# Performance work log

Hardware: AMD Instinct MI355X
Metric: run time of the kernel (lower is better)

## Reference

```python
import jax, jax.numpy as jnp
import numpy as np

B, C, H, W = 4, 128, 64, 64


def setup_inputs() -> dict:
    key = jax.random.key(0)
    ks = jax.random.split(key, 7)
    s = 1.0 / np.sqrt(C)
    return {
        "x": jax.random.normal(ks[0], (B, C, H, W), dtype=jnp.float32),
        "Wq": jax.random.normal(ks[1], (C, C), dtype=jnp.float32) * s,
        "bq": jnp.zeros((C,), dtype=jnp.float32),
        "Wk": jax.random.normal(ks[2], (C, C), dtype=jnp.float32) * s,
        "bk": jnp.zeros((C,), dtype=jnp.float32),
        "Wv": jax.random.normal(ks[3], (C, C), dtype=jnp.float32) * s,
        "bv": jnp.zeros((C,), dtype=jnp.float32),
    }


def reference(x, Wq, bq, Wk, bk, Wv, bv):
    b, c, h, w = x.shape
    n = h * w
    scale = c ** (-0.5)
    # tokens: [B, N, C]
    xt = x.reshape(b, c, n).transpose(0, 2, 1)
    # 1x1 convs == per-token channel GEMMs (out[c'] = sum_c W[c',c] x[c] + b[c'])
    q = jnp.einsum("bnc,dc->bnd", xt, Wq) + bq  # [B, N, C]
    k = jnp.einsum("bnc,dc->bnd", xt, Wk) + bk  # [B, N, C]
    v = jnp.einsum("bnc,dc->bnd", xt, Wv) + bv  # [B, N, C]
    scores = jnp.einsum("bic,bjc->bij", q, k) * scale  # [B, N, N]
    attn = jax.nn.softmax(scores, axis=-1)
    out = jnp.einsum("bij,bjc->bic", attn, v)  # [B, N, C]
    return out.transpose(0, 2, 1).reshape(b, c, h, w)
```

## Files before the change

kernel.cpp:

```cpp
#include <hip/hip_runtime.h>
#include <hip/hip_bf16.h>


#define BATCH 4
#define CH    128
#define NTOK  4096
#define TK    64
#define SCALE 0.08838834764831845f
#define LOG2E 1.4426950408889634f
#define MFIX  16.0f

typedef __attribute__((ext_vector_type(8)))  short short8;
typedef __attribute__((ext_vector_type(4)))  float f32x4;
typedef __attribute__((ext_vector_type(16))) float f32x16;

static __device__ __forceinline__ unsigned short f2bf(float f) {
    __hip_bfloat16 h = (__hip_bfloat16)f;
    return *(const unsigned short*)&h;
}

static __device__ __forceinline__ unsigned cvt_pk_bf16(float lo, float hi) {
    unsigned r;
    asm("v_cvt_pk_bf16_f32 %0, %1, %2" : "=v"(r) : "v"(lo), "v"(hi));
    return r;
}

static __device__ __forceinline__ short8 pack_bf16x8(float4 a, float4 b) {
    union { unsigned u[4]; short8 s8; } f;
    f.u[0] = cvt_pk_bf16(a.x, a.y);
    f.u[1] = cvt_pk_bf16(a.z, a.w);
    f.u[2] = cvt_pk_bf16(b.x, b.y);
    f.u[3] = cvt_pk_bf16(b.z, b.w);
    return f.s8;
}

__global__ __launch_bounds__(256) void proj_mfma_kernel(
    const float* __restrict__ x,
    const float* __restrict__ Wq, const float* __restrict__ Wk,
    const float* __restrict__ Wv,
    const float* __restrict__ bq, const float* __restrict__ bk,
    const float* __restrict__ bv,
    unsigned short* __restrict__ q_ws, unsigned short* __restrict__ kf_ws,
    unsigned short* __restrict__ vt_ws)
{
    __shared__ __align__(16) unsigned short Wl[CH * CH];
    __shared__ __align__(16) unsigned short XsT[64 * CH];

    const int t    = threadIdx.x;
    const int w    = t >> 6;
    const int lane = t & 63;
    const int quad = lane >> 4;
    const int c16  = lane & 15;
    const int n0   = blockIdx.x * 64;
    const int b    = blockIdx.y;
    const int z    = blockIdx.z;
    const float* xb = x + (size_t)b * CH * NTOK;
    const float* wm = (z == 0) ? Wq : (z == 1) ? Wk : Wv;

    #pragma unroll
    for (int i = 0; i < 8; ++i) {
        const int f   = i * 256 + t;
        const int row = f >> 4;
        const int u   = f & 15;
        const float* src = wm + f * 8;
        const float4 a = *(const float4*)src;
        const float4 c = *(const float4*)(src + 4);
        *(short8*)&Wl[row * CH + ((u ^ (row & 15)) << 3)] = pack_bf16x8(a, c);
    }
    {
        const int tok = lane;
        #pragma unroll
        for (int cc = 0; cc < 4; ++cc) {
            const int cb = 32 * w + 8 * cc;
            float xv[8];
            #pragma unroll
            for (int j = 0; j < 8; ++j)
                xv[j] = xb[(size_t)(cb + j) * NTOK + n0 + tok];
            union { unsigned u[4]; short8 s8; } pk;
            #pragma unroll
            for (int j = 0; j < 4; ++j)
                pk.u[j] = cvt_pk_bf16(xv[2 * j], xv[2 * j + 1]);
            const int phys = ((cb >> 3) ^ (tok & 15));
            *(short8*)&XsT[tok * CH + phys * 8] = pk.s8;
        }
    }
    __syncthreads();

    if (z < 2) {
        const float* bias = (z == 0) ? bq : bk;
        const float mul = (z == 0) ? (SCALE * LOG2E) : 1.0f;
        short8 xa[4];
        #pragma unroll
        for (int ks = 0; ks < 4; ++ks)
            xa[ks] = *(const short8*)&XsT[(16 * w + c16) * CH + (((4 * ks + quad) ^ c16) << 3)];
        #pragma unroll
        for (int nt = 0; nt < 8; ++nt) {
            f32x4 a = (f32x4){0.f, 0.f, 0.f, 0.f};
            #pragma unroll
            for (int ks = 0; ks < 4; ++ks) {
                const short8 bf = *(const short8*)
                    &Wl[(16 * nt + c16) * CH + (((4 * ks + quad) ^ c16) << 3)];
                a = __builtin_amdgcn_mfma_f32_16x16x32_bf16(xa[ks], bf, a, 0, 0, 0);
            }
            const float bvv = bias[16 * nt + c16];
            #pragma unroll
            for (int r = 0; r < 4; ++r) {
                const int n = n0 + 16 * w + quad * 4 + r;
                if (z == 0) {
                    q_ws[((size_t)b * NTOK + n) * CH + 16 * nt + c16] =
                        f2bf((a[r] + bvv) * mul);
                } else {
                    const size_t idx =
                        (((size_t)b * (NTOK >> 5) + (n >> 5)) * 8 + nt) * 512
                        + ((n & 31) + 32 * (c16 >> 3)) * 8 + (c16 & 7);
                    kf_ws[idx] = f2bf(a[r] + bvv);
                }
            }
        }
    } else {
        #pragma unroll
        for (int nt = 0; nt < 4; ++nt) {
            short8 xbf[4];
            #pragma unroll
            for (int ks = 0; ks < 4; ++ks)
                xbf[ks] = *(const short8*)&XsT[(16 * nt + c16) * CH + (((4 * ks + quad) ^ c16) << 3)];
            #pragma unroll
            for (int mt = 0; mt < 2; ++mt) {
                const int crow16 = 16 * (2 * w + mt);
                f32x4 acc = (f32x4){0.f, 0.f, 0.f, 0.f};
                #pragma unroll
                for (int ks = 0; ks < 4; ++ks) {
                    const short8 wva = *(const short8*)
                        &Wl[(crow16 + c16) * CH + (((4 * ks + quad) ^ c16) << 3)];
                    acc = __builtin_amdgcn_mfma_f32_16x16x32_bf16(wva, xbf[ks], acc, 0, 0, 0);
                }
                #pragma unroll
                for (int r = 0; r < 4; ++r) {
                    const int crow = crow16 + quad * 4 + r;
                    vt_ws[((size_t)b * CH + crow) * NTOK + n0 + 16 * nt + c16] =
                        f2bf(acc[r] + bv[crow]);
                }
            }
        }
    }
}

template <int SPLIT>
__global__ __launch_bounds__(256, 2) void flash_attn_mfma(
    const unsigned short* __restrict__ q_ws,
    const unsigned short* __restrict__ kf_ws,
    const unsigned short* __restrict__ vt_ws,
    float* __restrict__ out,
    float* __restrict__ Op, float* __restrict__ l_p)
{
    __shared__ __align__(16) unsigned short VtU[2][CH * TK];

    const int t    = threadIdx.x;
    const int w    = t >> 6;
    const int lane = t & 63;
    const int half = lane >> 5;
    const int l32  = lane & 31;
    const int jc   = blockIdx.y;
    const int b    = blockIdx.z;
    const int n0   = blockIdx.x * 128;
    const int jbeg = jc * (NTOK / SPLIT);
    constexpr int NT = (NTOK / SPLIT) / TK;
    static_assert(NT >= 2, "need at least 2 tiles");

    const unsigned short* kg = kf_ws + (size_t)b * NTOK * CH;
    const unsigned short* vg = vt_ws + (size_t)b * CH * NTOK;

    short8 qa[8];
    {
        const unsigned short* qrow =
            q_ws + ((size_t)b * NTOK + n0 + 32 * w + l32) * CH;
        #pragma unroll
        for (int ks = 0; ks < 8; ++ks)
            qa[ks] = *(const short8*)(qrow + ks * 16 + half * 8);
    }

    f32x16 Oa[4];
    #pragma unroll
    for (int ct = 0; ct < 4; ++ct) Oa[ct] = (f32x16)(0.0f);
    float lsum = 0.f;

    const int vcl = lane >> 3, vu = lane & 7;

    auto V_DMA = [&](int buf, int jj) {
        #pragma unroll
        for (int ci = 0; ci < 4; ++ci) {
            const int c = 32 * w + 8 * ci + vcl;
            const int g = vu ^ (c & 7);
            const unsigned short* src = vg + (size_t)c * NTOK + jj + g * 8;
            __builtin_amdgcn_global_load_lds(
                (const __attribute__((address_space(1))) void*)src,
                (__attribute__((address_space(3))) void*)&VtU[buf][(32 * w + 8 * ci) * TK],
                16, 0, 0);
        }
    };

    short8 kf[2][8];
    auto KF_LOAD = [&](int jj) {
        const unsigned short* kb = kg + (size_t)(jj >> 5) * 8 * 512;
        #pragma unroll
        for (int kt = 0; kt < 2; ++kt)
            #pragma unroll
            for (int ks = 0; ks < 8; ++ks)
                kf[kt][ks] = *(const short8*)(kb + ((kt * 8 + ks) * 64 + lane) * 8);
    };

    V_DMA(0, jbeg);
    KF_LOAD(jbeg);

    int j0 = jbeg;
    for (int tt = 0; tt < NT; ++tt, j0 += TK) {
        const int cur = tt & 1;
        if (tt + 1 < NT) {
            V_DMA(cur ^ 1, j0 + TK);
            asm volatile("s_waitcnt vmcnt(8)" ::: "memory");
        } else {
            asm volatile("s_waitcnt vmcnt(0)" ::: "memory");
        }
        __builtin_amdgcn_sched_barrier(0);
        __builtin_amdgcn_s_barrier();
        __builtin_amdgcn_sched_barrier(0);

        f32x16 s[2];
        s[0] = (f32x16)(-MFIX);
        s[1] = (f32x16)(-MFIX);
        #pragma unroll
        for (int ks = 0; ks < 8; ++ks) {
            s[0] = __builtin_amdgcn_mfma_f32_32x32x16_bf16(kf[0][ks], qa[ks], s[0], 0, 0, 0);
            s[1] = __builtin_amdgcn_mfma_f32_32x32x16_bf16(kf[1][ks], qa[ks], s[1], 0, 0, 0);
        }
        __builtin_amdgcn_sched_barrier(0);
        if (tt + 1 < NT) KF_LOAD(j0 + TK);
        __builtin_amdgcn_sched_barrier(0);

        short8 pb[4];
        #pragma unroll
        for (int kt = 0; kt < 2; ++kt) {
            float p[16];
            #pragma unroll
            for (int r = 0; r < 16; ++r) p[r] = exp2f(s[kt][r]);
            float a0 = 0.f, a1 = 0.f, a2 = 0.f, a3 = 0.f;
            #pragma unroll
            for (int r = 0; r < 4; ++r) {
                a0 += p[r]; a1 += p[4 + r]; a2 += p[8 + r]; a3 += p[12 + r];
            }
            lsum += (a0 + a1) + (a2 + a3);
            unsigned wd[8];
            #pragma unroll
            for (int i = 0; i < 8; ++i) wd[i] = cvt_pk_bf16(p[2 * i], p[2 * i + 1]);
            auto r02 = __builtin_amdgcn_permlane32_swap(wd[0], wd[2], false, false);
            auto r13 = __builtin_amdgcn_permlane32_swap(wd[1], wd[3], false, false);
            auto r46 = __builtin_amdgcn_permlane32_swap(wd[4], wd[6], false, false);
            auto r57 = __builtin_amdgcn_permlane32_swap(wd[5], wd[7], false, false);
            union { unsigned u[4]; short8 s8; } f0, f1;
            f0.u[0] = r02[0]; f0.u[1] = r13[0]; f0.u[2] = r02[1]; f0.u[3] = r13[1];
            f1.u[0] = r46[0]; f1.u[1] = r57[0]; f1.u[2] = r46[1]; f1.u[3] = r57[1];
            pb[2 * kt + 0] = f0.s8;
            pb[2 * kt + 1] = f1.s8;
        }

        #pragma unroll
        for (int ks2 = 0; ks2 < 4; ++ks2) {
            #pragma unroll
            for (int ct = 0; ct < 4; ++ct) {
                const int ch = 32 * ct + l32;
                const int ph = (2 * ks2 + half) ^ (ch & 7);
                const short8 vf = *(const short8*)&VtU[cur][ch * TK + ph * 8];
                Oa[ct] = __builtin_amdgcn_mfma_f32_32x32x16_bf16(vf, pb[ks2], Oa[ct], 0, 0, 0);
            }
        }
        __builtin_amdgcn_sched_barrier(0);
        __builtin_amdgcn_s_barrier();
        __builtin_amdgcn_sched_barrier(0);
    }

    const float lt = lsum + __shfl_xor(lsum, 32);
    const int n = n0 + 32 * w + l32;

    if constexpr (SPLIT == 1) {
        const float inv = 1.0f / lt;
        #pragma unroll
        for (int ct = 0; ct < 4; ++ct) {
            #pragma unroll
            for (int r = 0; r < 16; ++r) {
                const int c = 32 * ct + (r & 3) + 8 * (r >> 2) + 4 * half;
                out[((size_t)b * CH + c) * NTOK + n] = Oa[ct][r] * inv;
            }
        }
    } else {
        const size_t chunk = (size_t)(b * SPLIT + jc);
        #pragma unroll
        for (int ct = 0; ct < 4; ++ct) {
            #pragma unroll
            for (int r = 0; r < 16; ++r) {
                const int c = 32 * ct + (r & 3) + 8 * (r >> 2) + 4 * half;
                Op[(chunk * CH + c) * NTOK + n] = Oa[ct][r];
            }
        }
        if (half == 0) l_p[chunk * NTOK + n] = lt;
    }
}

template <int SPLIT>
__global__ __launch_bounds__(256) void combine_kernel(
    const float* __restrict__ Op, const float* __restrict__ l_p,
    float* __restrict__ out)
{
    const int b = blockIdx.y;
    const size_t idx = ((size_t)blockIdx.x * 256 + threadIdx.x) * 4;
    const int c = (int)(idx >> 12);
    const int n = (int)(idx & (NTOK - 1));
    float4 acc = make_float4(0.f, 0.f, 0.f, 0.f);
    float4 den = make_float4(0.f, 0.f, 0.f, 0.f);
    #pragma unroll
    for (int j = 0; j < SPLIT; ++j) {
        const size_t chunk = (size_t)(b * SPLIT + j);
        const float4 o = *(const float4*)&Op[(chunk * CH + c) * NTOK + n];
        const float4 d = *(const float4*)&l_p[chunk * NTOK + n];
        acc.x += o.x; acc.y += o.y; acc.z += o.z; acc.w += o.w;
        den.x += d.x; den.y += d.y; den.z += d.z; den.w += d.w;
    }
    float4 r;
    r.x = acc.x / den.x; r.y = acc.y / den.y;
    r.z = acc.z / den.z; r.w = acc.w / den.w;
    *(float4*)&out[((size_t)b * CH * NTOK) + idx] = r;
}

extern "C" void kernel_launch(void* const* d_in, const int* in_sizes, int n_in,
                              void* d_out, int out_size, void* d_ws, size_t ws_size,
                              hipStream_t stream) {
    const float* x  = (const float*)d_in[0];
    const float* Wq = (const float*)d_in[1];
    const float* bq = (const float*)d_in[2];
    const float* Wk = (const float*)d_in[3];
    const float* bk = (const float*)d_in[4];
    const float* Wv = (const float*)d_in[5];
    const float* bv = (const float*)d_in[6];
    float* out = (float*)d_out;

    const size_t QKV = (size_t)BATCH * NTOK * CH;
    unsigned short* q_ws  = (unsigned short*)d_ws;
    unsigned short* kf_ws = q_ws + QKV;
    unsigned short* vt_ws = kf_ws + QKV;
    float* Op = (float*)(vt_ws + QKV);

    const size_t baseBytes = 3 * QKV * 2;
    auto needBytes = [&](size_t S) {
        return baseBytes + S * BATCH * NTOK * (size_t)(CH * 4 + 4);
    };

    dim3 gp(NTOK / 64, BATCH, 3);
    proj_mfma_kernel<<<gp, 256, 0, stream>>>(x, Wq, Wk, Wv, bq, bk, bv,
                                             q_ws, kf_ws, vt_ws);

    dim3 gc(CH * NTOK / 1024, BATCH);
    if (ws_size >= needBytes(4)) {
        float* l_p = Op + (size_t)4 * BATCH * NTOK * CH;
        dim3 ga(NTOK / 128, 4, BATCH);
        flash_attn_mfma<4><<<ga, 256, 0, stream>>>(q_ws, kf_ws, vt_ws, out, Op, l_p);
        combine_kernel<4><<<gc, 256, 0, stream>>>(Op, l_p, out);
    } else if (ws_size >= needBytes(2)) {
        float* l_p = Op + (size_t)2 * BATCH * NTOK * CH;
        dim3 ga(NTOK / 128, 2, BATCH);
        flash_attn_mfma<2><<<ga, 256, 0, stream>>>(q_ws, kf_ws, vt_ws, out, Op, l_p);
        combine_kernel<2><<<gc, 256, 0, stream>>>(Op, l_p, out);
    } else {
        dim3 ga(NTOK / 128, 1, BATCH);
        flash_attn_mfma<1><<<ga, 256, 0, stream>>>(q_ws, kf_ws, vt_ws, out,
                                                   nullptr, nullptr);
    }
}
```

Before: 128.6 us.

## Store V in MFMA-fragment layout and load directly to registers, drop LDS

The projection kernel now writes V in a pre-swizzled fragment layout that matches the MFMA operand order, so the attention kernel loads V fragments straight from global memory into registers. This removes the LDS double buffer, the DMA and both block barriers per tile. The tile size drops to 32 keys per iteration. The grid is flattened to 1D with a block-index remap that interleaves batches and splits, likely for L2/XCD locality, and the SPLIT=2 path is removed. In exchange, each wave now loads V separately with no sharing across waves, which raises global and L2 traffic, and there is less latency hiding without the explicit prefetch.

```diff
diff --git a/kernel.cpp b/kernel.cpp
--- a/kernel.cpp
+++ b/kernel.cpp
@@ -5,7 +5,6 @@
 #define BATCH 4
 #define CH    128
 #define NTOK  4096
-#define TK    64
 #define SCALE 0.08838834764831845f
 #define LOG2E 1.4426950408889634f
 #define MFIX  16.0f
@@ -41,7 +40,7 @@
     const float* __restrict__ bq, const float* __restrict__ bk,
     const float* __restrict__ bv,
     unsigned short* __restrict__ q_ws, unsigned short* __restrict__ kf_ws,
-    unsigned short* __restrict__ vt_ws)
+    unsigned short* __restrict__ vf_ws)
 {
     __shared__ __align__(16) unsigned short Wl[CH * CH];
     __shared__ __align__(16) unsigned short XsT[64 * CH];
@@ -136,9 +135,13 @@
                 }
                 #pragma unroll
                 for (int r = 0; r < 4; ++r) {
-                    const int crow = crow16 + quad * 4 + r;
-                    vt_ws[((size_t)b * CH + crow) * NTOK + n0 + 16 * nt + c16] =
-                        f2bf(acc[r] + bv[crow]);
+                    const int ch  = crow16 + quad * 4 + r;
+                    const int tok = n0 + 16 * nt + c16;
+                    const size_t idx =
+                        ((((size_t)b * (NTOK >> 5) + (tok >> 5)) * 2
+                          + ((tok >> 4) & 1)) * 4 + (ch >> 5)) * 512
+                        + ((ch & 31) + 32 * ((tok >> 3) & 1)) * 8 + (tok & 7);
+                    vf_ws[idx] = f2bf(acc[r] + bv[ch]);
                 }
             }
         }
@@ -149,26 +152,36 @@
 __global__ __launch_bounds__(256, 2) void flash_attn_mfma(
     const unsigned short* __restrict__ q_ws,
     const unsigned short* __restrict__ kf_ws,
-    const unsigned short* __restrict__ vt_ws,
+    const unsigned short* __restrict__ vf_ws,
     float* __restrict__ out,
     float* __restrict__ Op, float* __restrict__ l_p)
 {
-    __shared__ __align__(16) unsigned short VtU[2][CH * TK];
-
     const int t    = threadIdx.x;
     const int w    = t >> 6;
     const int lane = t & 63;
     const int half = lane >> 5;
     const int l32  = lane & 31;
-    const int jc   = blockIdx.y;
-    const int b    = blockIdx.z;
-    const int n0   = blockIdx.x * 128;
+
+    int xx, jc, b;
+    if constexpr (SPLIT == 4) {
+        const int bid = blockIdx.x;
+        b = (bid & 7) >> 1;
+        const int sub = ((bid & 1) << 6) | (bid >> 3);
+        jc = sub >> 5;
+        xx = sub & 31;
+    } else {
+        const int bid = blockIdx.x;
+        xx = bid & 31;
+        jc = (bid >> 5) % SPLIT;
+        b  = bid / (32 * SPLIT);
+    }
+
+    const int n0   = xx * 128;
     const int jbeg = jc * (NTOK / SPLIT);
-    constexpr int NT = (NTOK / SPLIT) / TK;
-    static_assert(NT >= 2, "need at least 2 tiles");
+    constexpr int NT2 = (NTOK / SPLIT) / 32;
 
     const unsigned short* kg = kf_ws + (size_t)b * NTOK * CH;
-    const unsigned short* vg = vt_ws + (size_t)b * CH * NTOK;
+    const unsigned short* vg = vf_ws + (size_t)b * NTOK * CH;
 
     short8 qa[8];
     {
@@ -184,71 +197,48 @@
     for (int ct = 0; ct < 4; ++ct) Oa[ct] = (f32x16)(0.0f);
     float lsum = 0.f;
 
-    const int vcl = lane >> 3, vu = lane & 7;
-
-    auto V_DMA = [&](int buf, int jj) {
-        #pragma unroll
-        for (int ci = 0; ci < 4; ++ci) {
-            const int c = 32 * w + 8 * ci + vcl;
-            const int g = vu ^ (c & 7);
-            const unsigned short* src = vg + (size_t)c * NTOK + jj + g * 8;
-            __builtin_amdgcn_global_load_lds(
-                (const __attribute__((address_space(1))) void*)src,
-                (__attribute__((address_space(3))) void*)&VtU[buf][(32 * w + 8 * ci) * TK],
-                16, 0, 0);
-        }
+    short8 kf[8];
+    auto KF_LOAD = [&](int jj) {
+        const unsigned short* kb = kg + (size_t)(jj >> 5) * (8 * 512);
+        #pragma unroll
+        for (int ks = 0; ks < 8; ++ks)
+            kf[ks] = *(const short8*)(kb + (ks * 64 + lane) * 8);
     };
 
-    short8 kf[2][8];
-    auto KF_LOAD = [&](int jj) {
-        const unsigned short* kb = kg + (size_t)(jj >> 5) * 8 * 512;
-        #pragma unroll
-        for (int kt = 0; kt < 2; ++kt)
-            #pragma unroll
-            for (int ks = 0; ks < 8; ++ks)
-                kf[kt][ks] = *(const short8*)(kb + ((kt * 8 + ks) * 64 + lane) * 8);
-    };
-
-    V_DMA(0, jbeg);
     KF_LOAD(jbeg);
 
     int j0 = jbeg;
-    for (int tt = 0; tt < NT; ++tt, j0 += TK) {
-        const int cur = tt & 1;
-        if (tt + 1 < NT) {
-            V_DMA(cur ^ 1, j0 + TK);
-            asm volatile("s_waitcnt vmcnt(8)" ::: "memory");
-        } else {
-            asm volatile("s_waitcnt vmcnt(0)" ::: "memory");
-        }
-        __builtin_amdgcn_sched_barrier(0);
-        __builtin_amdgcn_s_barrier();
-        __builtin_amdgcn_sched_barrier(0);
-
-        f32x16 s[2];
-        s[0] = (f32x16)(-MFIX);
-        s[1] = (f32x16)(-MFIX);
-        #pragma unroll
-        for (int ks = 0; ks < 8; ++ks) {
-            s[0] = __builtin_amdgcn_mfma_f32_32x32x16_bf16(kf[0][ks], qa[ks], s[0], 0, 0, 0);
-            s[1] = __builtin_amdgcn_mfma_f32_32x32x16_bf16(kf[1][ks], qa[ks], s[1], 0, 0, 0);
-        }
-        __builtin_amdgcn_sched_barrier(0);
-        if (tt + 1 < NT) KF_LOAD(j0 + TK);
-        __builtin_amdgcn_sched_barrier(0);
-
-        short8 pb[4];
-        #pragma unroll
-        for (int kt = 0; kt < 2; ++kt) {
-            float p[16];
-            #pragma unroll
-            for (int r = 0; r < 16; ++r) p[r] = exp2f(s[kt][r]);
+    for (int tt = 0; tt < NT2; ++tt, j0 += 32) {
+        f32x16 s = (f32x16)(-MFIX);
+        #pragma unroll
+        for (int ks = 0; ks < 8; ++ks)
+            s = __builtin_amdgcn_mfma_f32_32x32x16_bf16(kf[ks], qa[ks], s, 0, 0, 0);
+
+        short8 vfA[4], vfB[4];
+        {
+            const unsigned short* vb = vg + (size_t)(j0 >> 5) * (8 * 512);
+            #pragma unroll
+            for (int ct = 0; ct < 4; ++ct)
+                vfA[ct] = *(const short8*)(vb + ((0 * 4 + ct) * 64 + lane) * 8);
+            #pragma unroll
+            for (int ct = 0; ct < 4; ++ct)
+                vfB[ct] = *(const short8*)(vb + ((1 * 4 + ct) * 64 + lane) * 8);
+        }
+        if (tt + 1 < NT2) KF_LOAD(j0 + 32);
+
+        float p[16];
+        #pragma unroll
+        for (int r = 0; r < 16; ++r) p[r] = exp2f(s[r]);
+        {
             float a0 = 0.f, a1 = 0.f, a2 = 0.f, a3 = 0.f;
             #pragma unroll
             for (int r = 0; r < 4; ++r) {
                 a0 += p[r]; a1 += p[4 + r]; a2 += p[8 + r]; a3 += p[12 + r];
             }
             lsum += (a0 + a1) + (a2 + a3);
+        }
+        short8 pb0, pb1;
+        {
             unsigned wd[8];
             #pragma unroll
             for (int i = 0; i < 8; ++i) wd[i] = cvt_pk_bf16(p[2 * i], p[2 * i + 1]);
@@ -259,23 +249,16 @@
             union { unsigned u[4]; short8 s8; } f0, f1;
             f0.u[0] = r02[0]; f0.u[1] = r13[0]; f0.u[2] = r02[1]; f0.u[3] = r13[1];
             f1.u[0] = r46[0]; f1.u[1] = r57[0]; f1.u[2] = r46[1]; f1.u[3] = r57[1];
-            pb[2 * kt + 0] = f0.s8;
-            pb[2 * kt + 1] = f1.s8;
-        }
-
-        #pragma unroll
-        for (int ks2 = 0; ks2 < 4; ++ks2) {
-            #pragma unroll
-            for (int ct = 0; ct < 4; ++ct) {
-                const int ch = 32 * ct + l32;
-                const int ph = (2 * ks2 + half) ^ (ch & 7);
-                const short8 vf = *(const short8*)&VtU[cur][ch * TK + ph * 8];
-                Oa[ct] = __builtin_amdgcn_mfma_f32_32x32x16_bf16(vf, pb[ks2], Oa[ct], 0, 0, 0);
-            }
-        }
-        __builtin_amdgcn_sched_barrier(0);
-        __builtin_amdgcn_s_barrier();
-        __builtin_amdgcn_sched_barrier(0);
+            pb0 = f0.s8;
+            pb1 = f1.s8;
+        }
+
+        #pragma unroll
+        for (int ct = 0; ct < 4; ++ct)
+            Oa[ct] = __builtin_amdgcn_mfma_f32_32x32x16_bf16(vfA[ct], pb0, Oa[ct], 0, 0, 0);
+        #pragma unroll
+        for (int ct = 0; ct < 4; ++ct)
+            Oa[ct] = __builtin_amdgcn_mfma_f32_32x32x16_bf16(vfB[ct], pb1, Oa[ct], 0, 0, 0);
     }
 
     const float lt = lsum + __shfl_xor(lsum, 32);
@@ -345,8 +328,8 @@
     const size_t QKV = (size_t)BATCH * NTOK * CH;
     unsigned short* q_ws  = (unsigned short*)d_ws;
     unsigned short* kf_ws = q_ws + QKV;
-    unsigned short* vt_ws = kf_ws + QKV;
-    float* Op = (float*)(vt_ws + QKV);
+    unsigned short* vf_ws = kf_ws + QKV;
+    float* Op = (float*)(vf_ws + QKV);
 
     const size_t baseBytes = 3 * QKV * 2;
     auto needBytes = [&](size_t S) {
@@ -355,22 +338,16 @@
 
     dim3 gp(NTOK / 64, BATCH, 3);
     proj_mfma_kernel<<<gp, 256, 0, stream>>>(x, Wq, Wk, Wv, bq, bk, bv,
-                                             q_ws, kf_ws, vt_ws);
+                                             q_ws, kf_ws, vf_ws);
 
     dim3 gc(CH * NTOK / 1024, BATCH);
     if (ws_size >= needBytes(4)) {
         float* l_p = Op + (size_t)4 * BATCH * NTOK * CH;
-        dim3 ga(NTOK / 128, 4, BATCH);
-        flash_attn_mfma<4><<<ga, 256, 0, stream>>>(q_ws, kf_ws, vt_ws, out, Op, l_p);
+        flash_attn_mfma<4><<<dim3(32 * 4 * BATCH), 256, 0, stream>>>(
+            q_ws, kf_ws, vf_ws, out, Op, l_p);
         combine_kernel<4><<<gc, 256, 0, stream>>>(Op, l_p, out);
-    } else if (ws_size >= needBytes(2)) {
-        float* l_p = Op + (size_t)2 * BATCH * NTOK * CH;
-        dim3 ga(NTOK / 128, 2, BATCH);
-        flash_attn_mfma<2><<<ga, 256, 0, stream>>>(q_ws, kf_ws, vt_ws, out, Op, l_p);
-        combine_kernel<2><<<gc, 256, 0, stream>>>(Op, l_p, out);
     } else {
-        dim3 ga(NTOK / 128, 1, BATCH);
-        flash_attn_mfma<1><<<ga, 256, 0, stream>>>(q_ws, kf_ws, vt_ws, out,
-                                                   nullptr, nullptr);
-    }
-}
+        flash_attn_mfma<1><<<dim3(32 * BATCH), 256, 0, stream>>>(
+            q_ws, kf_ws, vf_ws, out, nullptr, nullptr);
+    }
+}
```

Result: no change. 126.5 us, median of 2 (-1.7%).
